# Kernel tuning notes

Measured on AMD Instinct MI355X. Metric: run time of the kernel, lower is better.

Reference implementation:

```python
import jax, jax.numpy as jnp
import numpy as np

B, T, F, H = 64, 512, 512, 1024

def setup_inputs() -> dict:
    key = jax.random.key(0)
    k1, k2, k3, k4 = jax.random.split(key, 4)
    std = 1.0 / np.sqrt(H)
    return {
        "x": jax.random.normal(k1, (B, T, F), dtype=jnp.float32),
        "U": jax.random.normal(k2, (F, 4 * H), dtype=jnp.float32) * (1.0 / np.sqrt(F)),
        "W": jax.random.normal(k3, (H, 4 * H), dtype=jnp.float32) * std,
        "b": jax.random.uniform(k4, (4 * H,), dtype=jnp.float32, minval=-std, maxval=std),
    }

def reference(x, U, W, b):
    Bsz, Tlen, _ = x.shape
    Hs = W.shape[0]
    # Precompute input projection for all timesteps: [T, B, 4H]
    xU = jnp.einsum('btf,fg->tbg', x, U) + b
    h0 = jnp.zeros((Bsz, Hs), dtype=x.dtype)
    c0 = jnp.zeros((Bsz, Hs), dtype=x.dtype)

    def step(carry, xu_t):
        h_t, c_t = carry
        gates = xu_t + h_t @ W  # [B, 4H]
        f_t = jax.nn.sigmoid(gates[:, :Hs])
        i_t = jax.nn.sigmoid(gates[:, Hs:2 * Hs])
        o_t = jax.nn.sigmoid(gates[:, 2 * Hs:3 * Hs])
        c_tilde = jax.nn.sigmoid(gates[:, 3 * Hs:])  # faithful: original uses sigmoid here
        c_t = f_t * c_t + i_t * c_tilde
        h_t = o_t * jnp.tanh(c_t)
        return (h_t, c_t), h_t

    (h_T, c_T), hs = jax.lax.scan(step, (h0, c0), xU)
    hidden_seq = jnp.transpose(hs, (1, 0, 2))  # [B, T, H]
    return hidden_seq, h_T, c_T
```

## Files before the change

kernel.cpp:

```cpp
#include <hip/hip_runtime.h>


#define Bz 64
#define Tz 512
#define Fz 512
#define Hz 1024
#define ROWP16 1544
#define ROWP64 386
#define NBLK 256
#define NTHR 256

typedef unsigned short u16;
typedef unsigned int u32;
typedef unsigned long long u64;
typedef __attribute__((ext_vector_type(8))) short bf16x8;
typedef __attribute__((ext_vector_type(4))) float f32x4;

__device__ __forceinline__ u16 f2bf(float f) {
    union { float f; unsigned u; } v; v.f = f;
    unsigned r = v.u + 0x7FFFu + ((v.u >> 16) & 1u);
    return (u16)(r >> 16);
}
__device__ __forceinline__ float fast_sigmoid(float x) {
    return 1.0f / (1.0f + __expf(-x));
}
__device__ __forceinline__ float fast_tanh(float x) {
    float e = __expf(2.0f * x);
    return 1.0f - 2.0f / (e + 1.0f);
}

__global__ __launch_bounds__(256) void conv_x_kernel(const float* __restrict__ x,
                                                     u16* __restrict__ xb) {
    size_t i = (size_t)blockIdx.x * 256 + threadIdx.x;
    float4 v = ((const float4*)x)[i];
    ushort4 o;
    o.x = f2bf(v.x); o.y = f2bf(v.y); o.z = f2bf(v.z); o.w = f2bf(v.w);
    ((ushort4*)xb)[i] = o;
}

__global__ __launch_bounds__(256) void transpose_tile_kernel(const float* __restrict__ src,
                                                             u16* __restrict__ dst,
                                                             int K, int N) {
    __shared__ u16 tile[32][33];
    const int ntk = K >> 5;
    const int tk = blockIdx.x % ntk;
    const int tn = blockIdx.x / ntk;
    const int c = threadIdx.x & 31;
    const int r0 = threadIdx.x >> 5;
#pragma unroll
    for (int rr = 0; rr < 32; rr += 8) {
        const int r = r0 + rr;
        tile[r][c] = f2bf(src[(size_t)(tk * 32 + r) * N + tn * 32 + c]);
    }
    __syncthreads();
#pragma unroll
    for (int rr = 0; rr < 32; rr += 8) {
        const int r = r0 + rr;
        dst[(size_t)(tn * 32 + r) * K + tk * 32 + c] = tile[c][r];
    }
}

__global__ __launch_bounds__(256) void init_state_kernel(u32* __restrict__ h0,
                                                         u32* __restrict__ flags) {
    int i = blockIdx.x * 256 + threadIdx.x;
    h0[i] = 0u;
    if (i < 256) flags[i] = 0u;
}

__global__ __launch_bounds__(NTHR, 1) void lstm_persist(
    const u16* __restrict__ xb,
    const u16* __restrict__ UT,
    const u16* __restrict__ WT,
    const float* __restrict__ bias,
    u64* __restrict__ h0,
    u64* __restrict__ h1,
    float* __restrict__ out,
    u32* __restrict__ flags) {

    __shared__ __align__(16) u16 albuf[16 * ROWP16];
    __shared__ float gbuf[4 * 16 * 16];

    const int tid = threadIdx.x;
    const int w = tid >> 6;
    const int l = tid & 63;
    const int lr = l & 15;
    const int lk = l >> 4;
    const int bg = blockIdx.x >> 6;
    const int jg = blockIdx.x & 63;
    const int mbase = bg * 16;
    const int jbase = jg * 16;
    const int n = w * Hz + jbase + lr;

    bf16x8 bw[48];
    {
        const u16* Ub = UT + (size_t)n * Fz + lk * 8;
        const u16* Wb = WT + (size_t)n * Hz + lk * 8;
#pragma unroll
        for (int kb = 0; kb < 16; ++kb) bw[kb] = *(const bf16x8*)(Ub + kb * 32);
#pragma unroll
        for (int kb = 0; kb < 32; ++kb) bw[16 + kb] = *(const bf16x8*)(Wb + kb * 32);
    }
    const float bv = bias[n];

    const int ml_e = tid >> 4;
    const int jj_e = tid & 15;
    const int m_e = mbase + ml_e;
    const int j_e = jbase + jj_e;
    float creg = 0.0f;

    const size_t OFF_HT = (size_t)Bz * Tz * Hz;
    const size_t OFF_CT = OFF_HT + (size_t)Bz * Hz;

    const u32* __restrict__ flg = flags + bg * 64;
    u64* albuf64 = (u64*)albuf;

    bf16x8 tx[4];
#pragma unroll
    for (int it = 0; it < 4; ++it) {
        int idx = it * NTHR + tid;
        int ml = idx >> 6, ci = idx & 63;
        tx[it] = *(const bf16x8*)(xb + ((size_t)(mbase + ml) * Tz + 0) * Fz + ci * 8);
    }

#pragma unroll 1
    for (int t = 0; t < Tz; ++t) {
        const u64* __restrict__ hin  = (t & 1) ? h1 : h0;
        u64* __restrict__ hout       = (t & 1) ? h0 : h1;

#pragma unroll
        for (int it = 0; it < 4; ++it) {
            int idx = it * NTHR + tid;
            int ml = idx >> 6, ci = idx & 63;
            *(bf16x8*)(albuf + ml * ROWP16 + ci * 8) = tx[it];
        }
        __syncthreads();

        f32x4 a0 = {0.f,0.f,0.f,0.f}, a1 = a0, a2 = a0, a3 = a0;
        {
            const u16* abase = albuf + lr * ROWP16 + lk * 8;
#pragma unroll
            for (int kb = 0; kb < 16; kb += 4) {
                a0 = __builtin_amdgcn_mfma_f32_16x16x32_bf16(*(const bf16x8*)(abase + (kb+0)*32), bw[kb+0], a0, 0,0,0);
                a1 = __builtin_amdgcn_mfma_f32_16x16x32_bf16(*(const bf16x8*)(abase + (kb+1)*32), bw[kb+1], a1, 0,0,0);
                a2 = __builtin_amdgcn_mfma_f32_16x16x32_bf16(*(const bf16x8*)(abase + (kb+2)*32), bw[kb+2], a2, 0,0,0);
                a3 = __builtin_amdgcn_mfma_f32_16x16x32_bf16(*(const bf16x8*)(abase + (kb+3)*32), bw[kb+3], a3, 0,0,0);
            }
        }

        if (t) {
            const unsigned tgt = (unsigned)t;
            for (;;) {
                u32 v = __hip_atomic_load(flg + l, __ATOMIC_RELAXED,
                                          __HIP_MEMORY_SCOPE_AGENT);
                if (__all((int)(v >= tgt))) break;
            }
        }

        {
            u64 hv[16];
            const u64* hsrc = hin + (size_t)mbase * 256;
#pragma unroll
            for (int r = 0; r < 16; ++r)
                hv[r] = __hip_atomic_load(hsrc + r * NTHR + tid, __ATOMIC_RELAXED,
                                          __HIP_MEMORY_SCOPE_AGENT);
#pragma unroll
            for (int r = 0; r < 16; ++r) {
                int idx = r * NTHR + tid;
                int ml = idx >> 8, ci = idx & 255;
                albuf64[ml * ROWP64 + 128 + ci] = hv[r];
            }
        }
        __syncthreads();

        {
            const u16* abase = albuf + lr * ROWP16 + 512 + lk * 8;
#pragma unroll
            for (int kb = 0; kb < 32; kb += 4) {
                a0 = __builtin_amdgcn_mfma_f32_16x16x32_bf16(*(const bf16x8*)(abase + (kb+0)*32), bw[16+kb+0], a0, 0,0,0);
                a1 = __builtin_amdgcn_mfma_f32_16x16x32_bf16(*(const bf16x8*)(abase + (kb+1)*32), bw[16+kb+1], a1, 0,0,0);
                a2 = __builtin_amdgcn_mfma_f32_16x16x32_bf16(*(const bf16x8*)(abase + (kb+2)*32), bw[16+kb+2], a2, 0,0,0);
                a3 = __builtin_amdgcn_mfma_f32_16x16x32_bf16(*(const bf16x8*)(abase + (kb+3)*32), bw[16+kb+3], a3, 0,0,0);
            }
        }
        f32x4 acc = (a0 + a1) + (a2 + a3);

#pragma unroll
        for (int i = 0; i < 4; ++i)
            gbuf[w * 256 + (lk * 4 + i) * 16 + lr] = acc[i] + bv;
        __syncthreads();

        float hn, cn;
        {
            float fg = fast_sigmoid(gbuf[tid]);
            float ig = fast_sigmoid(gbuf[256 + tid]);
            float og = fast_sigmoid(gbuf[512 + tid]);
            float ct = fast_sigmoid(gbuf[768 + tid]);
            cn = fg * creg + ig * ct;
            creg = cn;
            hn = og * fast_tanh(cn);
            float hn1 = __shfl_xor(hn, 1);
            u32 p01 = ((u32)f2bf(hn1) << 16) | (u32)f2bf(hn);
            u32 p23 = __shfl_xor(p01, 2);
            if (!(jj_e & 3)) {
                u64 pk = ((u64)p23 << 32) | (u64)p01;
                __hip_atomic_store(hout + (size_t)m_e * 256 + (j_e >> 2), pk,
                                   __ATOMIC_RELAXED, __HIP_MEMORY_SCOPE_AGENT);
            }
        }

        if (t != Tz - 1) {
            __syncthreads();
            if (tid == 0)
                __hip_atomic_store((u32*)flg + jg, (u32)(t + 1),
                                   __ATOMIC_RELAXED, __HIP_MEMORY_SCOPE_AGENT);
        }

        out[((size_t)m_e * Tz + t) * Hz + j_e] = hn;
        if (t == Tz - 1) {
            out[OFF_HT + (size_t)m_e * Hz + j_e] = hn;
            out[OFF_CT + (size_t)m_e * Hz + j_e] = cn;
        } else {
#pragma unroll
            for (int it = 0; it < 4; ++it) {
                int idx = it * NTHR + tid;
                int ml = idx >> 6, ci = idx & 63;
                tx[it] = *(const bf16x8*)(xb + ((size_t)(mbase + ml) * Tz + (t + 1)) * Fz + ci * 8);
            }
        }
    }
}

extern "C" void kernel_launch(void* const* d_in, const int* in_sizes, int n_in,
                              void* d_out, int out_size, void* d_ws, size_t ws_size,
                              hipStream_t stream) {
    const float* x    = (const float*)d_in[0];
    const float* U    = (const float*)d_in[1];
    const float* W    = (const float*)d_in[2];
    const float* bias = (const float*)d_in[3];
    float* out = (float*)d_out;
    char* ws = (char*)d_ws;

    u16* xb    = (u16*)(ws + 0);
    u16* UT    = (u16*)(ws + 33554432);
    u16* WT    = (u16*)(ws + 37748736);
    u64* h0    = (u64*)(ws + 46137344);
    u64* h1    = (u64*)(ws + 46268416);
    u32* flags = (u32*)(ws + 46399488);

    conv_x_kernel<<<16384, 256, 0, stream>>>(x, xb);
    transpose_tile_kernel<<<2048, 256, 0, stream>>>(U, UT, 512, 4096);
    transpose_tile_kernel<<<4096, 256, 0, stream>>>(W, WT, 1024, 4096);
    init_state_kernel<<<128, 256, 0, stream>>>((u32*)h0, flags);

    lstm_persist<<<NBLK, NTHR, 0, stream>>>(xb, UT, WT, bias, h0, h1, out, flags);
}
```

Before: 1.537 ms.

## Replace flag-based step sync with sentinel-polled hidden-state ring buffer

Result: slower. 1.600 ms (+4.2%).

```diff
diff --git a/kernel.cpp b/kernel.cpp
--- a/kernel.cpp
+++ b/kernel.cpp
@@ -9,6 +9,7 @@
 #define ROWP64 386
 #define NBLK 256
 #define NTHR 256
+#define SENT 0xFFFFFFFFFFFFFFFFull
 
 typedef unsigned short u16;
 typedef unsigned int u32;
@@ -60,11 +61,9 @@
     }
 }
 
-__global__ __launch_bounds__(256) void init_state_kernel(u32* __restrict__ h0,
-                                                         u32* __restrict__ flags) {
+__global__ __launch_bounds__(256) void init_state_kernel(u64* __restrict__ hbuf) {
     int i = blockIdx.x * 256 + threadIdx.x;
-    h0[i] = 0u;
-    if (i < 256) flags[i] = 0u;
+    hbuf[i] = SENT;
 }
 
 __global__ __launch_bounds__(NTHR, 1) void lstm_persist(
@@ -72,10 +71,8 @@
     const u16* __restrict__ UT,
     const u16* __restrict__ WT,
     const float* __restrict__ bias,
-    u64* __restrict__ h0,
-    u64* __restrict__ h1,
-    float* __restrict__ out,
-    u32* __restrict__ flags) {
+    u64* __restrict__ hbuf,
+    float* __restrict__ out) {
 
     __shared__ __align__(16) u16 albuf[16 * ROWP16];
     __shared__ float gbuf[4 * 16 * 16];
@@ -111,8 +108,8 @@
     const size_t OFF_HT = (size_t)Bz * Tz * Hz;
     const size_t OFF_CT = OFF_HT + (size_t)Bz * Hz;
 
-    const u32* __restrict__ flg = flags + bg * 64;
     u64* albuf64 = (u64*)albuf;
+    const size_t myq = (size_t)m_e * 256 + (j_e >> 2);
 
     bf16x8 tx[4];
 #pragma unroll
@@ -124,9 +121,6 @@
 
 #pragma unroll 1
     for (int t = 0; t < Tz; ++t) {
-        const u64* __restrict__ hin  = (t & 1) ? h1 : h0;
-        u64* __restrict__ hout       = (t & 1) ? h0 : h1;
-
 #pragma unroll
         for (int it = 0; it < 4; ++it) {
             int idx = it * NTHR + tid;
@@ -148,31 +142,31 @@
         }
 
         if (t) {
-            const unsigned tgt = (unsigned)t;
-            for (;;) {
-                u32 v = __hip_atomic_load(flg + l, __ATOMIC_RELAXED,
-                                          __HIP_MEMORY_SCOPE_AGENT);
-                if (__all((int)(v >= tgt))) break;
-            }
-        }
-
-        {
+            const u64* hsrc = hbuf + (((size_t)(t - 1) & 3) << 14) + (size_t)mbase * 256;
             u64 hv[16];
-            const u64* hsrc = hin + (size_t)mbase * 256;
+            unsigned mask = 0xFFFFu;
 #pragma unroll
             for (int r = 0; r < 16; ++r)
                 hv[r] = __hip_atomic_load(hsrc + r * NTHR + tid, __ATOMIC_RELAXED,
                                           __HIP_MEMORY_SCOPE_AGENT);
 #pragma unroll
-            for (int r = 0; r < 16; ++r) {
-                int idx = r * NTHR + tid;
-                int ml = idx >> 8, ci = idx & 255;
-                albuf64[ml * ROWP64 + 128 + ci] = hv[r];
-            }
-        }
-        __syncthreads();
-
-        {
+            for (int r = 0; r < 16; ++r)
+                if (hv[r] != SENT) mask &= ~(1u << r);
+            while (mask) {
+#pragma unroll
+                for (int r = 0; r < 16; ++r)
+                    if (mask & (1u << r))
+                        hv[r] = __hip_atomic_load(hsrc + r * NTHR + tid, __ATOMIC_RELAXED,
+                                                  __HIP_MEMORY_SCOPE_AGENT);
+#pragma unroll
+                for (int r = 0; r < 16; ++r)
+                    if (hv[r] != SENT) mask &= ~(1u << r);
+            }
+#pragma unroll
+            for (int r = 0; r < 16; ++r)
+                albuf64[r * ROWP64 + 128 + tid] = hv[r];
+            __syncthreads();
+
             const u16* abase = albuf + lr * ROWP16 + 512 + lk * 8;
 #pragma unroll
             for (int kb = 0; kb < 32; kb += 4) {
@@ -203,16 +197,11 @@
             u32 p23 = __shfl_xor(p01, 2);
             if (!(jj_e & 3)) {
                 u64 pk = ((u64)p23 << 32) | (u64)p01;
-                __hip_atomic_store(hout + (size_t)m_e * 256 + (j_e >> 2), pk,
+                __hip_atomic_store(hbuf + (((size_t)t & 3) << 14) + myq, pk,
                                    __ATOMIC_RELAXED, __HIP_MEMORY_SCOPE_AGENT);
-            }
-        }
-
-        if (t != Tz - 1) {
-            __syncthreads();
-            if (tid == 0)
-                __hip_atomic_store((u32*)flg + jg, (u32)(t + 1),
+                __hip_atomic_store(hbuf + (((size_t)(t + 2) & 3) << 14) + myq, SENT,
                                    __ATOMIC_RELAXED, __HIP_MEMORY_SCOPE_AGENT);
+            }
         }
 
         out[((size_t)m_e * Tz + t) * Hz + j_e] = hn;
@@ -240,17 +229,15 @@
     float* out = (float*)d_out;
     char* ws = (char*)d_ws;
 
-    u16* xb    = (u16*)(ws + 0);
-    u16* UT    = (u16*)(ws + 33554432);
-    u16* WT    = (u16*)(ws + 37748736);
-    u64* h0    = (u64*)(ws + 46137344);
-    u64* h1    = (u64*)(ws + 46268416);
-    u32* flags = (u32*)(ws + 46399488);
+    u16* xb   = (u16*)(ws + 0);
+    u16* UT   = (u16*)(ws + 33554432);
+    u16* WT   = (u16*)(ws + 37748736);
+    u64* hbuf = (u64*)(ws + 46137344);
 
     conv_x_kernel<<<16384, 256, 0, stream>>>(x, xb);
     transpose_tile_kernel<<<2048, 256, 0, stream>>>(U, UT, 512, 4096);
     transpose_tile_kernel<<<4096, 256, 0, stream>>>(W, WT, 1024, 4096);
-    init_state_kernel<<<128, 256, 0, stream>>>((u32*)h0, flags);
-
-    lstm_persist<<<NBLK, NTHR, 0, stream>>>(xb, UT, WT, bias, h0, h1, out, flags);
-}
+    init_state_kernel<<<256, 256, 0, stream>>>(hbuf);
+
+    lstm_persist<<<NBLK, NTHR, 0, stream>>>(xb, UT, WT, bias, hbuf, out);
+}
```

## Split the per-step GEMM K dimension across two wave groups in 512-thread blocks

Applied to the files above, without the earlier changes.

Measured after the change: 1.473 ms. -4.1%, faster.

```diff
diff --git a/kernel.cpp b/kernel.cpp
--- a/kernel.cpp
+++ b/kernel.cpp
@@ -8,7 +8,7 @@
 #define ROWP16 1544
 #define ROWP64 386
 #define NBLK 256
-#define NTHR 256
+#define NTHR 512
 
 typedef unsigned short u16;
 typedef unsigned int u32;
@@ -78,10 +78,12 @@
     u32* __restrict__ flags) {
 
     __shared__ __align__(16) u16 albuf[16 * ROWP16];
-    __shared__ float gbuf[4 * 16 * 16];
+    __shared__ float gbuf[2][4 * 16 * 17];
 
     const int tid = threadIdx.x;
     const int w = tid >> 6;
+    const int g = w & 3;
+    const int kh = w >> 2;
     const int l = tid & 63;
     const int lr = l & 15;
     const int lk = l >> 4;
@@ -89,24 +91,26 @@
     const int jg = blockIdx.x & 63;
     const int mbase = bg * 16;
     const int jbase = jg * 16;
-    const int n = w * Hz + jbase + lr;
-
-    bf16x8 bw[48];
+    const int n = g * Hz + jbase + lr;
+
+    bf16x8 bwU[8], bwW[16];
     {
-        const u16* Ub = UT + (size_t)n * Fz + lk * 8;
-        const u16* Wb = WT + (size_t)n * Hz + lk * 8;
-#pragma unroll
-        for (int kb = 0; kb < 16; ++kb) bw[kb] = *(const bf16x8*)(Ub + kb * 32);
-#pragma unroll
-        for (int kb = 0; kb < 32; ++kb) bw[16 + kb] = *(const bf16x8*)(Wb + kb * 32);
-    }
-    const float bv = bias[n];
-
-    const int ml_e = tid >> 4;
+        const u16* Ub = UT + (size_t)n * Fz + kh * 256 + lk * 8;
+        const u16* Wb = WT + (size_t)n * Hz + kh * 512 + lk * 8;
+#pragma unroll
+        for (int kb = 0; kb < 8; ++kb)  bwU[kb] = *(const bf16x8*)(Ub + kb * 32);
+#pragma unroll
+        for (int kb = 0; kb < 16; ++kb) bwW[kb] = *(const bf16x8*)(Wb + kb * 32);
+    }
+
+    const int ml_e = (tid & 255) >> 4;
     const int jj_e = tid & 15;
     const int m_e = mbase + ml_e;
     const int j_e = jbase + jj_e;
     float creg = 0.0f;
+    float bv4[4];
+#pragma unroll
+    for (int gg = 0; gg < 4; ++gg) bv4[gg] = bias[gg * Hz + jbase + jj_e];
 
     const size_t OFF_HT = (size_t)Bz * Tz * Hz;
     const size_t OFF_CT = OFF_HT + (size_t)Bz * Hz;
@@ -114,9 +118,9 @@
     const u32* __restrict__ flg = flags + bg * 64;
     u64* albuf64 = (u64*)albuf;
 
-    bf16x8 tx[4];
-#pragma unroll
-    for (int it = 0; it < 4; ++it) {
+    bf16x8 tx[2];
+#pragma unroll
+    for (int it = 0; it < 2; ++it) {
         int idx = it * NTHR + tid;
         int ml = idx >> 6, ci = idx & 63;
         tx[it] = *(const bf16x8*)(xb + ((size_t)(mbase + ml) * Tz + 0) * Fz + ci * 8);
@@ -128,7 +132,7 @@
         u64* __restrict__ hout       = (t & 1) ? h0 : h1;
 
 #pragma unroll
-        for (int it = 0; it < 4; ++it) {
+        for (int it = 0; it < 2; ++it) {
             int idx = it * NTHR + tid;
             int ml = idx >> 6, ci = idx & 63;
             *(bf16x8*)(albuf + ml * ROWP16 + ci * 8) = tx[it];
@@ -137,13 +141,13 @@
 
         f32x4 a0 = {0.f,0.f,0.f,0.f}, a1 = a0, a2 = a0, a3 = a0;
         {
-            const u16* abase = albuf + lr * ROWP16 + lk * 8;
-#pragma unroll
-            for (int kb = 0; kb < 16; kb += 4) {
-                a0 = __builtin_amdgcn_mfma_f32_16x16x32_bf16(*(const bf16x8*)(abase + (kb+0)*32), bw[kb+0], a0, 0,0,0);
-                a1 = __builtin_amdgcn_mfma_f32_16x16x32_bf16(*(const bf16x8*)(abase + (kb+1)*32), bw[kb+1], a1, 0,0,0);
-                a2 = __builtin_amdgcn_mfma_f32_16x16x32_bf16(*(const bf16x8*)(abase + (kb+2)*32), bw[kb+2], a2, 0,0,0);
-                a3 = __builtin_amdgcn_mfma_f32_16x16x32_bf16(*(const bf16x8*)(abase + (kb+3)*32), bw[kb+3], a3, 0,0,0);
+            const u16* abase = albuf + lr * ROWP16 + kh * 256 + lk * 8;
+#pragma unroll
+            for (int kb = 0; kb < 8; kb += 4) {
+                a0 = __builtin_amdgcn_mfma_f32_16x16x32_bf16(*(const bf16x8*)(abase + (kb+0)*32), bwU[kb+0], a0, 0,0,0);
+                a1 = __builtin_amdgcn_mfma_f32_16x16x32_bf16(*(const bf16x8*)(abase + (kb+1)*32), bwU[kb+1], a1, 0,0,0);
+                a2 = __builtin_amdgcn_mfma_f32_16x16x32_bf16(*(const bf16x8*)(abase + (kb+2)*32), bwU[kb+2], a2, 0,0,0);
+                a3 = __builtin_amdgcn_mfma_f32_16x16x32_bf16(*(const bf16x8*)(abase + (kb+3)*32), bwU[kb+3], a3, 0,0,0);
             }
         }
 
@@ -157,14 +161,14 @@
         }
 
         {
-            u64 hv[16];
+            u64 hv[8];
             const u64* hsrc = hin + (size_t)mbase * 256;
 #pragma unroll
-            for (int r = 0; r < 16; ++r)
+            for (int r = 0; r < 8; ++r)
                 hv[r] = __hip_atomic_load(hsrc + r * NTHR + tid, __ATOMIC_RELAXED,
                                           __HIP_MEMORY_SCOPE_AGENT);
 #pragma unroll
-            for (int r = 0; r < 16; ++r) {
+            for (int r = 0; r < 8; ++r) {
                 int idx = r * NTHR + tid;
                 int ml = idx >> 8, ci = idx & 255;
                 albuf64[ml * ROWP64 + 128 + ci] = hv[r];
@@ -173,28 +177,29 @@
         __syncthreads();
 
         {
-            const u16* abase = albuf + lr * ROWP16 + 512 + lk * 8;
-#pragma unroll
-            for (int kb = 0; kb < 32; kb += 4) {
-                a0 = __builtin_amdgcn_mfma_f32_16x16x32_bf16(*(const bf16x8*)(abase + (kb+0)*32), bw[16+kb+0], a0, 0,0,0);
-                a1 = __builtin_amdgcn_mfma_f32_16x16x32_bf16(*(const bf16x8*)(abase + (kb+1)*32), bw[16+kb+1], a1, 0,0,0);
-                a2 = __builtin_amdgcn_mfma_f32_16x16x32_bf16(*(const bf16x8*)(abase + (kb+2)*32), bw[16+kb+2], a2, 0,0,0);
-                a3 = __builtin_amdgcn_mfma_f32_16x16x32_bf16(*(const bf16x8*)(abase + (kb+3)*32), bw[16+kb+3], a3, 0,0,0);
+            const u16* abase = albuf + lr * ROWP16 + 512 + kh * 512 + lk * 8;
+#pragma unroll
+            for (int kb = 0; kb < 16; kb += 4) {
+                a0 = __builtin_amdgcn_mfma_f32_16x16x32_bf16(*(const bf16x8*)(abase + (kb+0)*32), bwW[kb+0], a0, 0,0,0);
+                a1 = __builtin_amdgcn_mfma_f32_16x16x32_bf16(*(const bf16x8*)(abase + (kb+1)*32), bwW[kb+1], a1, 0,0,0);
+                a2 = __builtin_amdgcn_mfma_f32_16x16x32_bf16(*(const bf16x8*)(abase + (kb+2)*32), bwW[kb+2], a2, 0,0,0);
+                a3 = __builtin_amdgcn_mfma_f32_16x16x32_bf16(*(const bf16x8*)(abase + (kb+3)*32), bwW[kb+3], a3, 0,0,0);
             }
         }
         f32x4 acc = (a0 + a1) + (a2 + a3);
 
 #pragma unroll
         for (int i = 0; i < 4; ++i)
-            gbuf[w * 256 + (lk * 4 + i) * 16 + lr] = acc[i] + bv;
+            gbuf[kh][g * 272 + (lk * 4 + i) * 17 + lr] = acc[i];
         __syncthreads();
 
-        float hn, cn;
-        {
-            float fg = fast_sigmoid(gbuf[tid]);
-            float ig = fast_sigmoid(gbuf[256 + tid]);
-            float og = fast_sigmoid(gbuf[512 + tid]);
-            float ct = fast_sigmoid(gbuf[768 + tid]);
+        float hn = 0.0f, cn = 0.0f;
+        if (tid < 256) {
+            const int q = ml_e * 17 + jj_e;
+            float fg = fast_sigmoid(gbuf[0][q]        + gbuf[1][q]        + bv4[0]);
+            float ig = fast_sigmoid(gbuf[0][272 + q]  + gbuf[1][272 + q]  + bv4[1]);
+            float og = fast_sigmoid(gbuf[0][544 + q]  + gbuf[1][544 + q]  + bv4[2]);
+            float ct = fast_sigmoid(gbuf[0][816 + q]  + gbuf[1][816 + q]  + bv4[3]);
             cn = fg * creg + ig * ct;
             creg = cn;
             hn = og * fast_tanh(cn);
@@ -215,13 +220,16 @@
                                    __ATOMIC_RELAXED, __HIP_MEMORY_SCOPE_AGENT);
         }
 
-        out[((size_t)m_e * Tz + t) * Hz + j_e] = hn;
-        if (t == Tz - 1) {
-            out[OFF_HT + (size_t)m_e * Hz + j_e] = hn;
-            out[OFF_CT + (size_t)m_e * Hz + j_e] = cn;
-        } else {
-#pragma unroll
-            for (int it = 0; it < 4; ++it) {
+        if (tid < 256) {
+            out[((size_t)m_e * Tz + t) * Hz + j_e] = hn;
+            if (t == Tz - 1) {
+                out[OFF_HT + (size_t)m_e * Hz + j_e] = hn;
+                out[OFF_CT + (size_t)m_e * Hz + j_e] = cn;
+            }
+        }
+        if (t + 1 < Tz) {
+#pragma unroll
+            for (int it = 0; it < 2; ++it) {
                 int idx = it * NTHR + tid;
                 int ml = idx >> 6, ci = idx & 63;
                 tx[it] = *(const bf16x8*)(xb + ((size_t)(mbase + ml) * Tz + (t + 1)) * Fz + ci * 8);
```
